# Optimization experiments

Measured on AMD Instinct MI355X. Metric: run time of the kernel, lower is better.

Reference implementation:

```python
import jax, jax.numpy as jnp
import numpy as np
from jax import lax

GAMMA = 0.1


def setup_inputs() -> dict:
    key = jax.random.key(0)
    k1, k2 = jax.random.split(key)
    pred = jax.random.normal(k1, (64, 512), dtype=jnp.float32)
    target = jax.random.normal(k2, (64, 512), dtype=jnp.float32)
    return {"pred": pred, "target": target}


def _soft_dtw(pred, target, gamma=GAMMA):
    # pred, target: [B, L]
    B, L = pred.shape
    inf = jnp.float32(jnp.inf)
    # pairwise squared distances: [B, L, L]
    dist = (pred[:, :, None] - target[:, None, :]) ** 2

    def softmin3(r0, r1, r2):
        # -gamma * logsumexp(-r/gamma) over the 3 predecessors (stable)
        s = jnp.stack([r0, r1, r2], axis=-1)
        return -gamma * jax.nn.logsumexp(-s / gamma, axis=-1)

    # R[0, :] = [0, inf, inf, ...]  (row 0 of the (L+1)x(L+1) DP table)
    init_row = jnp.concatenate(
        [jnp.zeros((B, 1), jnp.float32), jnp.full((B, L), inf, jnp.float32)], axis=1
    )  # [B, L+1]

    def row_step(prev_row, d_row):
        # prev_row: R[i-1, :] of shape [B, L+1]; d_row: dist[:, i-1, :] of shape [B, L]
        r0s = prev_row[:, :-1].T  # R[i-1, j-1], [L, B]
        r1s = prev_row[:, 1:].T   # R[i-1, j],   [L, B]
        ds = d_row.T              # [L, B]

        def cell(r_left, inp):
            r0, r1, d = inp
            val = d + softmin3(r0, r1, r_left)
            return val, val

        _, vals = lax.scan(cell, jnp.full((B,), inf, jnp.float32), (r0s, r1s, ds))
        new_row = jnp.concatenate([jnp.full((B, 1), inf, jnp.float32), vals.T], axis=1)
        return new_row, None

    # scan over rows i = 1..L; dist reordered to [L, B, L]
    last_row, _ = lax.scan(row_step, init_row, jnp.swapaxes(dist, 0, 1))
    return last_row[:, -1].mean()  # R[:, L, L].mean()


def reference(pred, target):
    return _soft_dtw(pred, target)
```

## Files before the change

### kernel.cpp

```cpp
#include <hip/hip_runtime.h>

#define LSEQ 512
#define NB 64
#define NCHUNK 51

__device__ __forceinline__ float dpp_shr1_inj(float inj, float x) {
  return __int_as_float(__builtin_amdgcn_update_dpp(
      __float_as_int(inj), __float_as_int(x), 0x138, 0xF, 0xF, false));
}

__device__ __forceinline__ float rdlane(float x, int u) {
  return __int_as_float(__builtin_amdgcn_readlane(__float_as_int(x), u));
}

__device__ __forceinline__ float exp2_fast(float x) {
  const float xc = fmaxf(x, -126.0f);
  const float f = __builtin_fmaf(xc, 8388608.0f, 1065353216.0f);
  return __int_as_float((int)f);
}

__device__ __forceinline__ void renorm(float& d, float& e) {
  const int eb = __float_as_int(e);
  const int E = (eb >> 23) - 127;
  e = __int_as_float((eb & 0x007FFFFF) | 0x3F800000);
  d -= (float)E;
}

template <bool FULL>
__device__ __forceinline__ void chunk16(
    int cbase, const float* tgpad, const float2* ring2P, float2* ring2W,
    float p0, float p1, bool is_wr, int lane, float& v0d, float& v0e,
    float& v1d, float& v1e, float& r0d, float& r0e) {
  renorm(v0d, v0e);
  renorm(v1d, v1e);

  float tt[16];
  const int tb = 64 + cbase - lane;
#pragma unroll
  for (int k = 0; k < 16; ++k) tt[k] = tgpad[tb + k];

  const float2 rj = ring2P[(cbase + 1 + (lane & 15)) & 127];
  float sjd[16], sje[16];
#pragma unroll
  for (int k = 0; k < 16; ++k) {
    sjd[k] = rdlane(rj.x, k);
    sje[k] = rdlane(rj.y, k);
  }

  float vvd[16], vve[16];
#pragma unroll
  for (int u = 0; u < 16; ++u) {
    const float r1d = dpp_shr1_inj(sjd[u], v1d);
    const float r1e = dpp_shr1_inj(sje[u], v1e);
    const float tcu = tt[u];
    const float diff0 = p0 - tcu;
    const float M0 = fminf(fminf(r0d, r1d), v0d);
    const float d0 = __builtin_fmaf(diff0, diff0, M0);
    const float diff1 = p1 - tcu;
    const float M1 = fminf(fminf(v0d, d0), v1d);
    const float d1 = __builtin_fmaf(diff1, diff1, M1);
    const float x0 = exp2_fast(M0 - r0d);
    const float x1 = exp2_fast(M0 - r1d);
    const float x2 = exp2_fast(M0 - v0d);
    const float x3 = exp2_fast(M1 - v0d);
    const float x4 = exp2_fast(M1 - d0);
    const float x5 = exp2_fast(M1 - v1d);
    const float e0 = __builtin_fmaf(x2, v0e, __builtin_fmaf(x1, r1e, x0 * r0e));
    const float e1 = __builtin_fmaf(x5, v1e, __builtin_fmaf(x4, e0, x3 * v0e));
    vvd[u] = d1;
    vve[u] = e1;
    if (FULL) {
      v0d = d0; v0e = e0; v1d = d1; v1e = e1;
    } else {
      const int j = cbase + 1 + u - lane;
      const bool act = ((unsigned)(j - 1)) < (unsigned)LSEQ;
      v0d = act ? d0 : v0d; v0e = act ? e0 : v0e;
      v1d = act ? d1 : v1d; v1e = act ? e1 : v1e;
    }
    r0d = r1d;
    r0e = r1e;
  }

  if (is_wr) {
    const int j0 = cbase - 62;
#pragma unroll
    for (int k = 0; k < 16; ++k) {
      if (FULL || (((unsigned)(j0 + k - 1)) < (unsigned)LSEQ))
        ring2W[(j0 + k) & 127] = make_float2(vvd[k], vve[k]);
    }
  }
}

__global__ __launch_bounds__(256) void dtw_band(
    const float* __restrict__ pred, const float* __restrict__ target,
    float* __restrict__ part) {
  const int b = blockIdx.x;
  const int tid = threadIdx.x;
  const int w = tid >> 6;
  const int lane = tid & 63;
  const bool is_wr = (lane == 63) && (w < 3);

  __shared__ float tgpad[640];
  __shared__ float2 rings2[4][128];

  const float SC = 3.79828146f;
  const float2 pp = ((const float2*)(pred + b * LSEQ))[tid];
  const float p0 = pp.x * SC, p1 = pp.y * SC;
  const float2 tt = ((const float2*)(target + b * LSEQ))[tid];
  ((float2*)(tgpad + 64))[tid] = make_float2(tt.x * SC, tt.y * SC);
  if (tid < 64) {
    tgpad[tid] = 0.0f;
    tgpad[576 + tid] = 0.0f;
  }
  ((float2*)rings2)[tid] = make_float2(INFINITY, 1.0f);
  ((float2*)rings2)[tid + 256] = make_float2(INFINITY, 1.0f);

  const int lag = w * 80;
  const int cw0 = 5 * w;
  const float2* __restrict__ ring2P = rings2[w == 0 ? 3 : w - 1];
  float2* __restrict__ ring2W = rings2[w];

  float v0d = INFINITY, v0e = 1.0f;
  float v1d = INFINITY, v1e = 1.0f;
  float r0d = (tid == 0) ? 0.0f : INFINITY;
  float r0e = 1.0f;

  for (int c = 0; c < NCHUNK; ++c) {
    __syncthreads();
    if (c < cw0 || c > cw0 + 35) continue;
    const int cbase = 16 * c - lag;
    if (c >= cw0 + 4 && c <= cw0 + 31)
      chunk16<true>(cbase, tgpad, ring2P, ring2W, p0, p1, is_wr, lane, v0d,
                    v0e, v1d, v1e, r0d, r0e);
    else
      chunk16<false>(cbase, tgpad, ring2P, ring2W, p0, p1, is_wr, lane, v0d,
                     v0e, v1d, v1e, r0d, r0e);
  }

  if (tid == 255)
    part[b] = (v1d - __builtin_amdgcn_logf(v1e)) * 0.069314718f;
}

__global__ void dtw_reduce(const float* __restrict__ part,
                           float* __restrict__ out) {
  float v = part[threadIdx.x];
#pragma unroll
  for (int o = 32; o > 0; o >>= 1) v += __shfl_down(v, o);
  if (threadIdx.x == 0) out[0] = v * (1.0f / NB);
}

extern "C" void kernel_launch(void* const* d_in, const int* in_sizes, int n_in,
                              void* d_out, int out_size, void* d_ws,
                              size_t ws_size, hipStream_t stream) {
  const float* pred = (const float*)d_in[0];
  const float* target = (const float*)d_in[1];
  float* part = (float*)d_ws;

  dtw_band<<<NB, 256, 0, stream>>>(pred, target, part);
  dtw_reduce<<<1, 64, 0, stream>>>(part, (float*)d_out);
}
```

Before: 97.14 us.

## Replace deferred (value, scale) pair with per-cell fast log2 softmin

Each DP cell now holds a single log-domain value instead of a (value, mantissa-scale) pair. The softmin is computed per cell from min, median (fmed3) and max, using two fast exp2 calls and a bit-trick log2 approximation. This halves register state, DPP shuffles, readlanes and LDS ring traffic on the serial critical path. The price is an approximate log2 on every cell, whose error accumulates across the DP and may hurt accuracy.

```diff
diff --git a/kernel.cpp b/kernel.cpp
--- a/kernel.cpp
+++ b/kernel.cpp
@@ -18,75 +18,67 @@
   const float f = __builtin_fmaf(xc, 8388608.0f, 1065353216.0f);
   return __int_as_float((int)f);
 }
-
-__device__ __forceinline__ void renorm(float& d, float& e) {
-  const int eb = __float_as_int(e);
-  const int E = (eb >> 23) - 127;
-  e = __int_as_float((eb & 0x007FFFFF) | 0x3F800000);
-  d -= (float)E;
+__device__ __forceinline__ float log2_fast(float e) {
+  return (float)(__float_as_int(e) - 1065353216) * 1.1920929e-7f;
 }
 
 template <bool FULL>
 __device__ __forceinline__ void chunk16(
-    int cbase, const float* tgpad, const float2* ring2P, float2* ring2W,
-    float p0, float p1, bool is_wr, int lane, float& v0d, float& v0e,
-    float& v1d, float& v1e, float& r0d, float& r0e) {
-  renorm(v0d, v0e);
-  renorm(v1d, v1e);
-
+    int cbase, const float* tgpad, const float* ringP, float* ringW, float p0,
+    float p1, bool is_wr, int lane, float& v0, float& v1, float& r0) {
   float tt[16];
   const int tb = 64 + cbase - lane;
 #pragma unroll
   for (int k = 0; k < 16; ++k) tt[k] = tgpad[tb + k];
 
-  const float2 rj = ring2P[(cbase + 1 + (lane & 15)) & 127];
-  float sjd[16], sje[16];
+  const float rj = ringP[(cbase + 1 + (lane & 15)) & 127];
+  float sj[16];
 #pragma unroll
-  for (int k = 0; k < 16; ++k) {
-    sjd[k] = rdlane(rj.x, k);
-    sje[k] = rdlane(rj.y, k);
-  }
+  for (int k = 0; k < 16; ++k) sj[k] = rdlane(rj, k);
 
-  float vvd[16], vve[16];
+  float vv[16];
 #pragma unroll
   for (int u = 0; u < 16; ++u) {
-    const float r1d = dpp_shr1_inj(sjd[u], v1d);
-    const float r1e = dpp_shr1_inj(sje[u], v1e);
+    const float r1 = dpp_shr1_inj(sj[u], v1);
     const float tcu = tt[u];
     const float diff0 = p0 - tcu;
-    const float M0 = fminf(fminf(r0d, r1d), v0d);
-    const float d0 = __builtin_fmaf(diff0, diff0, M0);
+    const float M0 = fminf(fminf(r0, r1), v0);
+    const float md0 = __builtin_amdgcn_fmed3f(r0, r1, v0);
+    const float mx0 = fmaxf(fmaxf(r0, r1), v0);
+    const float e0 =
+        1.0f + (exp2_fast(M0 - md0) + exp2_fast(M0 - mx0));
+    const float d0 =
+        __builtin_fmaf(diff0, diff0, M0) - log2_fast(e0);
     const float diff1 = p1 - tcu;
-    const float M1 = fminf(fminf(v0d, d0), v1d);
-    const float d1 = __builtin_fmaf(diff1, diff1, M1);
-    const float x0 = exp2_fast(M0 - r0d);
-    const float x1 = exp2_fast(M0 - r1d);
-    const float x2 = exp2_fast(M0 - v0d);
-    const float x3 = exp2_fast(M1 - v0d);
-    const float x4 = exp2_fast(M1 - d0);
-    const float x5 = exp2_fast(M1 - v1d);
-    const float e0 = __builtin_fmaf(x2, v0e, __builtin_fmaf(x1, r1e, x0 * r0e));
-    const float e1 = __builtin_fmaf(x5, v1e, __builtin_fmaf(x4, e0, x3 * v0e));
-    vvd[u] = d1;
-    vve[u] = e1;
+    const float M1 = fminf(fminf(v0, d0), v1);
+    const float md1 = __builtin_amdgcn_fmed3f(v0, d0, v1);
+    const float mx1 = fmaxf(fmaxf(v0, d0), v1);
+    const float e1 =
+        1.0f + (exp2_fast(M1 - md1) + exp2_fast(M1 - mx1));
+    const float d1 =
+        __builtin_fmaf(diff1, diff1, M1) - log2_fast(e1);
+    vv[u] = d1;
     if (FULL) {
-      v0d = d0; v0e = e0; v1d = d1; v1e = e1;
+      v0 = d0;
+      v1 = d1;
     } else {
       const int j = cbase + 1 + u - lane;
       const bool act = ((unsigned)(j - 1)) < (unsigned)LSEQ;
-      v0d = act ? d0 : v0d; v0e = act ? e0 : v0e;
-      v1d = act ? d1 : v1d; v1e = act ? e1 : v1e;
+      v0 = act ? d0 : v0;
+      v1 = act ? d1 : v1;
     }
-    r0d = r1d;
-    r0e = r1e;
+    r0 = r1;
   }
 
   if (is_wr) {
     const int j0 = cbase - 62;
 #pragma unroll
-    for (int k = 0; k < 16; ++k) {
-      if (FULL || (((unsigned)(j0 + k - 1)) < (unsigned)LSEQ))
-        ring2W[(j0 + k) & 127] = make_float2(vvd[k], vve[k]);
+    for (int k = 0; k < 8; ++k) {
+      if (FULL || (((unsigned)(j0 + 2 * k - 1)) < (unsigned)LSEQ))
+        *(float2*)&ringW[(j0 + 2 * k) & 127] =
+            make_float2(vv[2 * k], vv[2 * k + 1]);
+      else if (((unsigned)(j0 + 2 * k)) < (unsigned)LSEQ)
+        ringW[(j0 + 2 * k + 1) & 127] = vv[2 * k + 1];
     }
   }
 }
@@ -101,7 +93,7 @@
   const bool is_wr = (lane == 63) && (w < 3);
 
   __shared__ float tgpad[640];
-  __shared__ float2 rings2[4][128];
+  __shared__ float rings[4][128];
 
   const float SC = 3.79828146f;
   const float2 pp = ((const float2*)(pred + b * LSEQ))[tid];
@@ -112,33 +104,31 @@
     tgpad[tid] = 0.0f;
     tgpad[576 + tid] = 0.0f;
   }
-  ((float2*)rings2)[tid] = make_float2(INFINITY, 1.0f);
-  ((float2*)rings2)[tid + 256] = make_float2(INFINITY, 1.0f);
+  ((float2*)rings)[tid] = make_float2(INFINITY, INFINITY);
 
   const int lag = w * 80;
   const int cw0 = 5 * w;
-  const float2* __restrict__ ring2P = rings2[w == 0 ? 3 : w - 1];
-  float2* __restrict__ ring2W = rings2[w];
+  const float* __restrict__ ringP = rings[w == 0 ? 3 : w - 1];
+  float* __restrict__ ringW = rings[w];
 
-  float v0d = INFINITY, v0e = 1.0f;
-  float v1d = INFINITY, v1e = 1.0f;
-  float r0d = (tid == 0) ? 0.0f : INFINITY;
-  float r0e = 1.0f;
+  float v0 = INFINITY;
+  float v1 = INFINITY;
+  float r0 = (tid == 0) ? 0.0f : INFINITY;
 
   for (int c = 0; c < NCHUNK; ++c) {
     __syncthreads();
     if (c < cw0 || c > cw0 + 35) continue;
     const int cbase = 16 * c - lag;
     if (c >= cw0 + 4 && c <= cw0 + 31)
-      chunk16<true>(cbase, tgpad, ring2P, ring2W, p0, p1, is_wr, lane, v0d,
-                    v0e, v1d, v1e, r0d, r0e);
+      chunk16<true>(cbase, tgpad, ringP, ringW, p0, p1, is_wr, lane, v0, v1,
+                    r0);
     else
-      chunk16<false>(cbase, tgpad, ring2P, ring2W, p0, p1, is_wr, lane, v0d,
-                     v0e, v1d, v1e, r0d, r0e);
+      chunk16<false>(cbase, tgpad, ringP, ringW, p0, p1, is_wr, lane, v0, v1,
+                     r0);
   }
 
   if (tid == 255)
-    part[b] = (v1d - __builtin_amdgcn_logf(v1e)) * 0.069314718f;
+    part[b] = v1 * 0.069314718f;
 }
 
 __global__ void dtw_reduce(const float* __restrict__ part,
```

New measurement: 85.08 us. 12.4% less time.
